# Optimization experiments

Measured on AMD Instinct MI355X. Metric: run time of the kernel, lower is better.

The kernel has to match this reference:

```python
import jax, jax.numpy as jnp
import numpy as np

# Class weights from __init__: total/len_i with len_0=1000, len_1=3000, len_2=6000
_TOTAL = 1000.0 + 3000.0 + 6000.0
CLASS_WEIGHTS = jnp.array([_TOTAL / 1000.0, _TOTAL / 3000.0, _TOTAL / 6000.0], dtype=jnp.float32)
NUM_CLASSES = 3
SMOOTHING = 0.1


def setup_inputs() -> dict:
    key = jax.random.key(0)
    k1, k2 = jax.random.split(key)
    N = 8388608
    pred = jax.random.normal(k1, (N, NUM_CLASSES), dtype=jnp.float32)
    label = jax.random.randint(k2, (N,), 0, NUM_CLASSES, dtype=jnp.int64)
    return {"pred": pred, "label": label}


def reference(pred, label):
    # log(softmax(pred)) computed stably; same math as -log(softmax) in the original
    logp = jax.nn.log_softmax(pred, axis=1)                      # [N, 3]
    one_hot = jax.nn.one_hot(label, NUM_CLASSES, dtype=pred.dtype)  # [N, 3]
    smoothed = (1.0 - SMOOTHING) * one_hot + SMOOTHING / NUM_CLASSES
    per_sample = -jnp.sum(logp * smoothed, axis=-1)              # [N]
    w = CLASS_WEIGHTS[label]                                     # gather per-sample weight
    return jnp.sum(per_sample * w) / pred.shape[0]
```

## Files before the change

kernel.cpp:

```cpp
#include <hip/hip_runtime.h>

#define NBLOCKS 2048
#define NTHREADS 256

typedef float __attribute__((ext_vector_type(4))) fx4;
typedef int   __attribute__((ext_vector_type(4))) ix4;

__device__ __forceinline__ float wave_reduce_sum(float v) {
    #pragma unroll
    for (int off = 32; off > 0; off >>= 1)
        v += __shfl_down(v, off, 64);
    return v;
}

__device__ __forceinline__ float sample_loss(float p0, float p1, float p2, int lab) {
    float m = fmaxf(p0, fmaxf(p1, p2));
    float e = __expf(p0 - m) + __expf(p1 - m) + __expf(p2 - m);
    float lse = m + __logf(e);
    float pl = (lab == 0) ? p0 : ((lab == 1) ? p1 : p2);
    float w  = (lab == 0) ? 10.0f : ((lab == 1) ? (10.0f / 3.0f) : (10.0f / 6.0f));
    float per = lse - (0.1f / 3.0f) * (p0 + p1 + p2) - 0.9f * pl;
    return w * per;
}

__global__ void __launch_bounds__(NTHREADS, 8)
ce_partial_kernel(const float* __restrict__ pred,
                  const int* __restrict__ label,
                  float* __restrict__ partials, int n) {
    int tid = blockIdx.x * blockDim.x + threadIdx.x;
    int nthreads = gridDim.x * blockDim.x;
    int groups = n >> 3;
    float acc = 0.0f;

    for (int g = tid; g < groups; g += nthreads) {
        const fx4* p4 = reinterpret_cast<const fx4*>(pred + (size_t)g * 24);
        const ix4* l4 = reinterpret_cast<const ix4*>(label) + (size_t)g * 2;
        fx4 a = p4[0];
        fx4 b = p4[1];
        fx4 c = p4[2];
        fx4 d = p4[3];
        fx4 e = p4[4];
        fx4 f = p4[5];
        ix4 l0 = l4[0];
        ix4 l1 = l4[1];
        acc += sample_loss(a.x, a.y, a.z, l0.x);
        acc += sample_loss(a.w, b.x, b.y, l0.y);
        acc += sample_loss(b.z, b.w, c.x, l0.z);
        acc += sample_loss(c.y, c.z, c.w, l0.w);
        acc += sample_loss(d.x, d.y, d.z, l1.x);
        acc += sample_loss(d.w, e.x, e.y, l1.y);
        acc += sample_loss(e.z, e.w, f.x, l1.z);
        acc += sample_loss(f.y, f.z, f.w, l1.w);
    }
    if (tid == 0) {
        for (int i = groups << 3; i < n; ++i) {
            acc += sample_loss(pred[(size_t)i * 3], pred[(size_t)i * 3 + 1],
                               pred[(size_t)i * 3 + 2], label[i]);
        }
    }

    __shared__ float sdata[NTHREADS / 64];
    float wsum = wave_reduce_sum(acc);
    int lane = threadIdx.x & 63;
    int wid  = threadIdx.x >> 6;
    if (lane == 0) sdata[wid] = wsum;
    __syncthreads();
    if (threadIdx.x == 0) {
        float s = 0.0f;
        #pragma unroll
        for (int i = 0; i < NTHREADS / 64; ++i) s += sdata[i];
        partials[blockIdx.x] = s;
    }
}

__global__ void __launch_bounds__(256)
ce_final_kernel(const float* __restrict__ partials, int nparts,
                float* __restrict__ out, float inv_n) {
    float acc = 0.0f;
    for (int i = threadIdx.x; i < nparts; i += 256) acc += partials[i];
    __shared__ float sdata[4];
    float wsum = wave_reduce_sum(acc);
    int lane = threadIdx.x & 63;
    int wid  = threadIdx.x >> 6;
    if (lane == 0) sdata[wid] = wsum;
    __syncthreads();
    if (threadIdx.x == 0) {
        float s = sdata[0] + sdata[1] + sdata[2] + sdata[3];
        out[0] = s * inv_n;
    }
}

extern "C" void kernel_launch(void* const* d_in, const int* in_sizes, int n_in,
                              void* d_out, int out_size, void* d_ws, size_t ws_size,
                              hipStream_t stream) {
    const float* pred = (const float*)d_in[0];
    const int* label = (const int*)d_in[1];
    int n = in_sizes[1];
    float* partials = (float*)d_ws;
    float* out = (float*)d_out;

    ce_partial_kernel<<<NBLOCKS, NTHREADS, 0, stream>>>(pred, label, partials, n);
    ce_final_kernel<<<1, 256, 0, stream>>>(partials, NBLOCKS, out, 1.0f / (float)n);
}
```

Measured before the change: 29.50 us.

## Fuse final reduction into single pass via fixed-point atomics and last-block detection

```diff
diff --git a/kernel.cpp b/kernel.cpp
--- a/kernel.cpp
+++ b/kernel.cpp
@@ -1,7 +1,8 @@
 #include <hip/hip_runtime.h>
 
 #define NBLOCKS 2048
-#define NTHREADS 256
+#define NTHREADS 512
+#define FIXED_SCALE 1048576.0f
 
 typedef float __attribute__((ext_vector_type(4))) fx4;
 typedef int   __attribute__((ext_vector_type(4))) ix4;
@@ -23,10 +24,12 @@
     return w * per;
 }
 
-__global__ void __launch_bounds__(NTHREADS, 8)
-ce_partial_kernel(const float* __restrict__ pred,
+__global__ void __launch_bounds__(NTHREADS)
+ce_onepass_kernel(const float* __restrict__ pred,
                   const int* __restrict__ label,
-                  float* __restrict__ partials, int n) {
+                  unsigned long long* __restrict__ total,
+                  unsigned long long* __restrict__ count,
+                  float* __restrict__ out, int n, float inv_n) {
     int tid = blockIdx.x * blockDim.x + threadIdx.x;
     int nthreads = gridDim.x * blockDim.x;
     int groups = n >> 3;
@@ -69,24 +72,20 @@
         float s = 0.0f;
         #pragma unroll
         for (int i = 0; i < NTHREADS / 64; ++i) s += sdata[i];
-        partials[blockIdx.x] = s;
-    }
-}
-
-__global__ void __launch_bounds__(256)
-ce_final_kernel(const float* __restrict__ partials, int nparts,
-                float* __restrict__ out, float inv_n) {
-    float acc = 0.0f;
-    for (int i = threadIdx.x; i < nparts; i += 256) acc += partials[i];
-    __shared__ float sdata[4];
-    float wsum = wave_reduce_sum(acc);
-    int lane = threadIdx.x & 63;
-    int wid  = threadIdx.x >> 6;
-    if (lane == 0) sdata[wid] = wsum;
-    __syncthreads();
-    if (threadIdx.x == 0) {
-        float s = sdata[0] + sdata[1] + sdata[2] + sdata[3];
-        out[0] = s * inv_n;
+        long long fx = llrintf(s * FIXED_SCALE);
+        unsigned long long oldt =
+            __hip_atomic_fetch_add(total, (unsigned long long)fx,
+                                   __ATOMIC_RELAXED, __HIP_MEMORY_SCOPE_AGENT);
+        unsigned long long bump = 1ull + (oldt >> 63);
+        unsigned long long oldc =
+            __hip_atomic_fetch_add(count, bump,
+                                   __ATOMIC_RELAXED, __HIP_MEMORY_SCOPE_AGENT);
+        if (oldc == (unsigned long long)(gridDim.x - 1)) {
+            unsigned long long tot =
+                __hip_atomic_fetch_add(total, 0ull,
+                                       __ATOMIC_RELAXED, __HIP_MEMORY_SCOPE_AGENT);
+            out[0] = (float)(long long)tot * (inv_n / FIXED_SCALE);
+        }
     }
 }
 
@@ -96,9 +95,11 @@
     const float* pred = (const float*)d_in[0];
     const int* label = (const int*)d_in[1];
     int n = in_sizes[1];
-    float* partials = (float*)d_ws;
+    unsigned long long* total = (unsigned long long*)d_ws;
+    unsigned long long* count = total + 1;
     float* out = (float*)d_out;
 
-    ce_partial_kernel<<<NBLOCKS, NTHREADS, 0, stream>>>(pred, label, partials, n);
-    ce_final_kernel<<<1, 256, 0, stream>>>(partials, NBLOCKS, out, 1.0f / (float)n);
+    (void)hipMemsetAsync(d_ws, 0, 2 * sizeof(unsigned long long), stream);
+    ce_onepass_kernel<<<NBLOCKS, NTHREADS, 0, stream>>>(pred, label, total, count,
+                                                        out, n, 1.0f / (float)n);
 }
```

After: 67.28 us. +128.1%, slower.
